# Optimization experiments

Measured on AMD Instinct MI355X. Metric: run time of the kernel, lower is better.

The kernel has to match this reference:

```python
import jax, jax.numpy as jnp
import numpy as np

B, S, D, H = 2, 2048, 1024, 16
DK = D // H


def setup_inputs() -> dict:
    key = jax.random.key(0)
    ks = jax.random.split(key, 6)
    scale = 1.0 / np.sqrt(D)
    return {
        "x": jax.random.normal(ks[0], (B, S, D), dtype=jnp.float32),
        "q": jax.random.normal(ks[1], (B, S, D), dtype=jnp.float32),
        "k": jax.random.normal(ks[2], (B, S, D), dtype=jnp.float32),
        "v": jax.random.normal(ks[3], (B, S, D), dtype=jnp.float32),
        "mask": jnp.ones((B, 1, S, S), dtype=jnp.int32),
        "Wq": jax.random.normal(ks[4], (D, D), dtype=jnp.float32) * scale,
        "Wo": jax.random.normal(ks[5], (D, D), dtype=jnp.float32) * scale,
    }


def reference(x, q, k, v, mask, Wq, Wo):
    b = x.shape[0]
    # NOTE: source projects q, k, v ALL through Wq (Wk/Wv unused in forward).
    def proj(t):
        # [b, s, D] -> [b, H, s, DK]   (nn.Linear: t @ W.T)
        return (t @ Wq.T).reshape(b, -1, H, DK).transpose(0, 2, 1, 3)

    query, key_, value = proj(q), proj(k), proj(v)
    # [b, H, Sq, Sk]
    scores = jnp.einsum("bhqd,bhkd->bhqk", query, key_) / np.sqrt(DK)
    scores = jnp.where(mask == 0, jnp.float32(1e-9), scores)
    attn = jax.nn.softmax(scores, axis=-1)
    out = jnp.einsum("bhqk,bhkd->bhqd", attn, value)  # [b, H, Sq, DK]
    out = out.transpose(0, 2, 1, 3).reshape(b, -1, D)
    return out @ Wo.T
```

## Files before the change

kernel.cpp:

```cpp
#include <hip/hip_runtime.h>

#define SEQ  2048
#define DDIM 1024
#define NH   16
#define DK   64

typedef _Float16 half8  __attribute__((ext_vector_type(8)));
typedef _Float16 half4v __attribute__((ext_vector_type(4)));
typedef float    floatx4 __attribute__((ext_vector_type(4)));

__device__ __forceinline__ void load_lds16(const void* g, void* l) {
  __builtin_amdgcn_global_load_lds(
      (const __attribute__((address_space(1))) void*)g,
      (__attribute__((address_space(3))) void*)l, 16, 0, 0);
}

__device__ __forceinline__ float fast_exp2(float x) {
#if __has_builtin(__builtin_amdgcn_exp2f)
  return __builtin_amdgcn_exp2f(x);
#else
  return exp2f(x);
#endif
}

__global__ __launch_bounds__(256) void cvt_kernel(
    const float* __restrict__ q, const float* __restrict__ k,
    const float* __restrict__ v, const float* __restrict__ Wq,
    const float* __restrict__ Wo, _Float16* __restrict__ ws) {
  long t = (long)blockIdx.x * 256 + threadIdx.x;
  long base = t * 4;
  const float* src;
  long off;
  if (base < 12582912L) {
    int which = (int)(base >> 22);
    src = which == 0 ? q : (which == 1 ? k : v);
    off = base & 4194303L;
  } else if (base < 13631488L) {
    src = Wq; off = base - 12582912L;
  } else {
    src = Wo; off = base - 13631488L;
  }
  float4 f = *(const float4*)(src + off);
  half4v h;
  h[0] = (_Float16)f.x; h[1] = (_Float16)f.y;
  h[2] = (_Float16)f.z; h[3] = (_Float16)f.w;
  *(half4v*)(ws + base) = h;
}

__device__ __forceinline__ void gemm128_core(
    const _Float16* __restrict__ A, const _Float16* __restrict__ B,
    int m0, int n0, _Float16* As, _Float16* Bs, floatx4 (&acc)[4][4]) {
  const int tid = threadIdx.x;
  const int lane = tid & 63, w = tid >> 6;
  const int wm = w >> 1, wn = w & 1;
  const int quad = lane >> 4, l15 = lane & 15;
  const int srow = lane >> 2, schunk = lane & 3;

#pragma unroll
  for (int i = 0; i < 4; ++i)
#pragma unroll
    for (int j = 0; j < 4; ++j)
#pragma unroll
      for (int r = 0; r < 4; ++r) acc[i][j][r] = 0.f;

  for (int k0 = 0; k0 < 1024; k0 += 32) {
    __syncthreads();
#pragma unroll
    for (int ii = 0; ii < 2; ++ii) {
      int rA = w * 32 + ii * 16 + srow;
      load_lds16(A + (long)(m0 + rA) * 1024 + k0 + schunk * 8,
                 As + (w * 32 + ii * 16) * 32);
      load_lds16(B + (long)(n0 + rA) * 1024 + k0 + schunk * 8,
                 Bs + (w * 32 + ii * 16) * 32);
    }
    __syncthreads();
    half8 af[4], bf[4];
#pragma unroll
    for (int f = 0; f < 4; ++f) {
      af[f] = *(const half8*)(As + (wm * 64 + f * 16 + l15) * 32 + quad * 8);
      bf[f] = *(const half8*)(Bs + (wn * 64 + f * 16 + l15) * 32 + quad * 8);
    }
#pragma unroll
    for (int i = 0; i < 4; ++i)
#pragma unroll
      for (int j = 0; j < 4; ++j)
        acc[i][j] = __builtin_amdgcn_mfma_f32_16x16x32_f16(af[i], bf[j],
                                                           acc[i][j], 0, 0, 0);
  }
}

__global__ __launch_bounds__(256) void proj_gemm(
    const _Float16* __restrict__ qkv16, const _Float16* __restrict__ w16,
    _Float16* __restrict__ Qp, _Float16* __restrict__ Kp,
    _Float16* __restrict__ Vt) {
  __shared__ __align__(16) _Float16 As[128 * 32];
  __shared__ __align__(16) _Float16 Bs[128 * 32];
  const int t = blockIdx.z;
  floatx4 acc[4][4];
  const int lane = threadIdx.x & 63, w = threadIdx.x >> 6;
  const int wm = w >> 1, wn = w & 1, quad = lane >> 4, l15 = lane & 15;

  if (t < 2) {
    const int m0 = blockIdx.y * 128, n0 = blockIdx.x * 128;
    gemm128_core(qkv16 + (long)t * 4194304, w16, m0, n0, As, Bs, acc);
#pragma unroll
    for (int i = 0; i < 4; ++i)
#pragma unroll
      for (int j = 0; j < 4; ++j)
#pragma unroll
        for (int r = 0; r < 4; ++r) {
          int m = m0 + wm * 64 + i * 16 + quad * 4 + r;
          int n = n0 + wn * 64 + j * 16 + l15;
          int b = m >> 11, s = m & 2047, h = n >> 6, dk = n & 63;
          long bh = b * NH + h;
          float val = acc[i][j][r];
          if (t == 0)
            Qp[(bh * SEQ + s) * DK + dk] = (_Float16)(val * 0.180336880f);
          else
            Kp[(bh * SEQ + s) * DK + dk] = (_Float16)val;
        }
  } else {
    const int m0 = blockIdx.x * 128, n0 = blockIdx.y * 128;
    gemm128_core(w16, qkv16 + 8388608L, m0, n0, As, Bs, acc);
#pragma unroll
    for (int i = 0; i < 4; ++i)
#pragma unroll
      for (int j = 0; j < 4; ++j)
#pragma unroll
        for (int r = 0; r < 4; ++r) {
          int m = m0 + wm * 64 + i * 16 + quad * 4 + r;
          int n = n0 + wn * 64 + j * 16 + l15;
          int h = m >> 6, dk = m & 63, b = n >> 11, s = n & 2047;
          Vt[(((long)b * NH + h) * DK + dk) * SEQ + s] = (_Float16)acc[i][j][r];
        }
  }
}

__global__ __launch_bounds__(256) void out_gemm(
    const _Float16* __restrict__ Aa, const _Float16* __restrict__ Bw,
    float* __restrict__ C) {
  __shared__ __align__(16) _Float16 As[128 * 32];
  __shared__ __align__(16) _Float16 Bs[128 * 32];
  const int m0 = blockIdx.y * 128, n0 = blockIdx.x * 128;
  floatx4 acc[4][4];
  gemm128_core(Aa, Bw, m0, n0, As, Bs, acc);

  const int lane = threadIdx.x & 63, w = threadIdx.x >> 6;
  const int wm = w >> 1, wn = w & 1, quad = lane >> 4, l15 = lane & 15;
#pragma unroll
  for (int i = 0; i < 4; ++i)
#pragma unroll
    for (int j = 0; j < 4; ++j)
#pragma unroll
      for (int r = 0; r < 4; ++r) {
        int m = m0 + wm * 64 + i * 16 + quad * 4 + r;
        int n = n0 + wn * 64 + j * 16 + l15;
        C[(long)m * 1024 + n] = acc[i][j][r];
      }
}

__global__ __launch_bounds__(256) void attn_kernel(
    const _Float16* __restrict__ Qp, const _Float16* __restrict__ Kp,
    const _Float16* __restrict__ Vt, _Float16* __restrict__ Oa) {
  __shared__ __align__(16) _Float16 smem[4096 * 3 + 4 * 16 * 68];
  _Float16* Qs = smem;
  _Float16* Ks = smem + 4096;
  _Float16* Vs = smem + 8192;
  const int tid = threadIdx.x;
  const int lane = tid & 63, w = tid >> 6;
  _Float16* Ps = smem + 12288 + w * (16 * 68);
  const int quad = lane >> 4, l15 = lane & 15;
  const int rl = lane >> 3, cc = lane & 7;
  const int bh = blockIdx.y;
  const int q0 = blockIdx.x * 64;
  const _Float16* Qb = Qp + (long)bh * (SEQ * DK);
  const _Float16* Kb = Kp + (long)bh * (SEQ * DK);
  const _Float16* Vb = Vt + (long)bh * (DK * SEQ);

#pragma unroll
  for (int ii = 0; ii < 2; ++ii) {
    int row = w * 16 + ii * 8 + rl;
    int gcc = cc ^ (row & 7);
    load_lds16(Qb + (long)(q0 + row) * DK + gcc * 8, Qs + (w * 16 + ii * 8) * 64);
  }
  __syncthreads();

  half8 qf[2];
#pragma unroll
  for (int ks = 0; ks < 2; ++ks) {
    int row = w * 16 + l15;
    int c = (ks * 4 + quad) ^ (row & 7);
    qf[ks] = *(const half8*)(Qs + row * 64 + c * 8);
  }

  floatx4 Oacc[4];
  floatx4 Dacc;
#pragma unroll
  for (int r = 0; r < 4; ++r) Dacc[r] = 0.f;
#pragma unroll
  for (int nt = 0; nt < 4; ++nt)
#pragma unroll
    for (int r = 0; r < 4; ++r) Oacc[nt][r] = 0.f;
  half8 ones;
#pragma unroll
  for (int i = 0; i < 8; ++i) ones[i] = (_Float16)1.0f;

  for (int kt = 0; kt < 32; ++kt) {
    const int k0 = kt * 64;
    __syncthreads();
#pragma unroll
    for (int ii = 0; ii < 2; ++ii) {
      int row = w * 16 + ii * 8 + rl;
      int gcc = cc ^ (row & 7);
      load_lds16(Kb + (long)(k0 + row) * DK + gcc * 8, Ks + (w * 16 + ii * 8) * 64);
      load_lds16(Vb + (long)row * SEQ + k0 + gcc * 8, Vs + (w * 16 + ii * 8) * 64);
    }
    __syncthreads();

    floatx4 Sacc[4];
#pragma unroll
    for (int nt = 0; nt < 4; ++nt)
#pragma unroll
      for (int r = 0; r < 4; ++r) Sacc[nt][r] = 0.f;
#pragma unroll
    for (int nt = 0; nt < 4; ++nt) {
#pragma unroll
      for (int ks = 0; ks < 2; ++ks) {
        int row = nt * 16 + l15;
        int c = (ks * 4 + quad) ^ (row & 7);
        half8 kf = *(const half8*)(Ks + row * 64 + c * 8);
        Sacc[nt] = __builtin_amdgcn_mfma_f32_16x16x32_f16(qf[ks], kf,
                                                          Sacc[nt], 0, 0, 0);
      }
    }

#pragma unroll
    for (int nt = 0; nt < 4; ++nt)
#pragma unroll
      for (int r = 0; r < 4; ++r) {
        float p = fast_exp2(Sacc[nt][r]);
        Ps[(quad * 4 + r) * 68 + nt * 16 + l15] = (_Float16)p;
      }

#pragma unroll
    for (int ks = 0; ks < 2; ++ks) {
      half8 pf = *(const half8*)(Ps + l15 * 68 + ks * 32 + quad * 8);
      Dacc = __builtin_amdgcn_mfma_f32_16x16x32_f16(pf, ones, Dacc, 0, 0, 0);
#pragma unroll
      for (int nt = 0; nt < 4; ++nt) {
        int row = nt * 16 + l15;
        int c = (ks * 4 + quad) ^ (row & 7);
        half8 vf = *(const half8*)(Vs + row * 64 + c * 8);
        Oacc[nt] = __builtin_amdgcn_mfma_f32_16x16x32_f16(pf, vf,
                                                          Oacc[nt], 0, 0, 0);
      }
    }
  }

  const int b = bh >> 4, h = bh & 15;
#pragma unroll
  for (int nt = 0; nt < 4; ++nt)
#pragma unroll
    for (int r = 0; r < 4; ++r) {
      float o = Oacc[nt][r] / Dacc[r];
      int srow = q0 + w * 16 + quad * 4 + r;
      int col = nt * 16 + l15;
      Oa[((long)b * SEQ + srow) * DDIM + h * DK + col] = (_Float16)o;
    }
}

extern "C" void kernel_launch(void* const* d_in, const int* in_sizes, int n_in,
                              void* d_out, int out_size, void* d_ws,
                              size_t ws_size, hipStream_t stream) {
  const float* q  = (const float*)d_in[1];
  const float* k  = (const float*)d_in[2];
  const float* v  = (const float*)d_in[3];
  const float* Wq = (const float*)d_in[5];
  const float* Wo = (const float*)d_in[6];
  float* out = (float*)d_out;

  _Float16* ws     = (_Float16*)d_ws;
  _Float16* qkv16  = ws;
  _Float16* wq16   = ws + 12582912;
  _Float16* wo16   = ws + 13631488;
  _Float16* Qp     = ws + 14680064;
  _Float16* Kp     = ws + 18874368;
  _Float16* Vt     = ws + 23068672;
  _Float16* attn16 = ws + 27262976;

  cvt_kernel<<<14336, 256, 0, stream>>>(q, k, v, Wq, Wo, ws);
  proj_gemm<<<dim3(8, 32, 3), 256, 0, stream>>>(qkv16, wq16, Qp, Kp, Vt);
  attn_kernel<<<dim3(32, 32), 256, 0, stream>>>(Qp, Kp, Vt, attn16);
  out_gemm<<<dim3(8, 32), 256, 0, stream>>>(attn16, wo16, out);
}
```

Baseline: 274.4 us.

## Retile GEMMs to 128x64 and restructure attention to keep P in registers

The projection and output GEMMs move from 128x128 to 128x64 tiles on a flattened 1D grid, doubling block count for better occupancy and load balance. The attention kernel drops to 128 threads, each wave handling 32 query rows. It computes S transposed so the exp'd probabilities feed the PV MFMA straight from registers (16x16x16), which removes the LDS round trip for P and the ones-matrix MFMA for the row sum. The epilogue stages the output through LDS so the global stores are coalesced 16-byte writes. These changes trade extra per-block setup and the removed GEMM B-tile reuse for lower LDS traffic and more parallelism.

```diff
diff --git a/kernel.cpp b/kernel.cpp
--- a/kernel.cpp
+++ b/kernel.cpp
@@ -47,17 +47,16 @@
   *(half4v*)(ws + base) = h;
 }
 
-__device__ __forceinline__ void gemm128_core(
+__device__ __forceinline__ void gemm_128x64_core(
     const _Float16* __restrict__ A, const _Float16* __restrict__ B,
-    int m0, int n0, _Float16* As, _Float16* Bs, floatx4 (&acc)[4][4]) {
+    int m0, int n0, _Float16* As, _Float16* Bs, floatx4 (&acc)[2][4]) {
   const int tid = threadIdx.x;
   const int lane = tid & 63, w = tid >> 6;
-  const int wm = w >> 1, wn = w & 1;
   const int quad = lane >> 4, l15 = lane & 15;
   const int srow = lane >> 2, schunk = lane & 3;
 
 #pragma unroll
-  for (int i = 0; i < 4; ++i)
+  for (int i = 0; i < 2; ++i)
 #pragma unroll
     for (int j = 0; j < 4; ++j)
 #pragma unroll
@@ -70,18 +69,22 @@
       int rA = w * 32 + ii * 16 + srow;
       load_lds16(A + (long)(m0 + rA) * 1024 + k0 + schunk * 8,
                  As + (w * 32 + ii * 16) * 32);
-      load_lds16(B + (long)(n0 + rA) * 1024 + k0 + schunk * 8,
-                 Bs + (w * 32 + ii * 16) * 32);
+    }
+    {
+      int rB = w * 16 + srow;
+      load_lds16(B + (long)(n0 + rB) * 1024 + k0 + schunk * 8,
+                 Bs + (w * 16) * 32);
     }
     __syncthreads();
-    half8 af[4], bf[4];
-#pragma unroll
-    for (int f = 0; f < 4; ++f) {
-      af[f] = *(const half8*)(As + (wm * 64 + f * 16 + l15) * 32 + quad * 8);
-      bf[f] = *(const half8*)(Bs + (wn * 64 + f * 16 + l15) * 32 + quad * 8);
-    }
-#pragma unroll
-    for (int i = 0; i < 4; ++i)
+    half8 af[2], bf[4];
+#pragma unroll
+    for (int i = 0; i < 2; ++i)
+      af[i] = *(const half8*)(As + (w * 32 + i * 16 + l15) * 32 + quad * 8);
+#pragma unroll
+    for (int j = 0; j < 4; ++j)
+      bf[j] = *(const half8*)(Bs + (j * 16 + l15) * 32 + quad * 8);
+#pragma unroll
+    for (int i = 0; i < 2; ++i)
 #pragma unroll
       for (int j = 0; j < 4; ++j)
         acc[i][j] = __builtin_amdgcn_mfma_f32_16x16x32_f16(af[i], bf[j],
@@ -94,23 +97,25 @@
     _Float16* __restrict__ Qp, _Float16* __restrict__ Kp,
     _Float16* __restrict__ Vt) {
   __shared__ __align__(16) _Float16 As[128 * 32];
-  __shared__ __align__(16) _Float16 Bs[128 * 32];
-  const int t = blockIdx.z;
-  floatx4 acc[4][4];
+  __shared__ __align__(16) _Float16 Bs[64 * 32];
+  const int bid = blockIdx.x;
+  floatx4 acc[2][4];
   const int lane = threadIdx.x & 63, w = threadIdx.x >> 6;
-  const int wm = w >> 1, wn = w & 1, quad = lane >> 4, l15 = lane & 15;
-
-  if (t < 2) {
-    const int m0 = blockIdx.y * 128, n0 = blockIdx.x * 128;
-    gemm128_core(qkv16 + (long)t * 4194304, w16, m0, n0, As, Bs, acc);
-#pragma unroll
-    for (int i = 0; i < 4; ++i)
+  const int quad = lane >> 4, l15 = lane & 15;
+
+  if (bid < 1024) {
+    const int t = bid >> 9;
+    const int local = bid & 511;
+    const int m0 = (local >> 4) * 128, n0 = (local & 15) * 64;
+    gemm_128x64_core(qkv16 + (long)t * 4194304, w16, m0, n0, As, Bs, acc);
+#pragma unroll
+    for (int i = 0; i < 2; ++i)
 #pragma unroll
       for (int j = 0; j < 4; ++j)
 #pragma unroll
         for (int r = 0; r < 4; ++r) {
-          int m = m0 + wm * 64 + i * 16 + quad * 4 + r;
-          int n = n0 + wn * 64 + j * 16 + l15;
+          int m = m0 + w * 32 + i * 16 + quad * 4 + r;
+          int n = n0 + j * 16 + l15;
           int b = m >> 11, s = m & 2047, h = n >> 6, dk = n & 63;
           long bh = b * NH + h;
           float val = acc[i][j][r];
@@ -120,16 +125,18 @@
             Kp[(bh * SEQ + s) * DK + dk] = (_Float16)val;
         }
   } else {
-    const int m0 = blockIdx.x * 128, n0 = blockIdx.y * 128;
-    gemm128_core(w16, qkv16 + 8388608L, m0, n0, As, Bs, acc);
-#pragma unroll
-    for (int i = 0; i < 4; ++i)
+    const int local = bid - 1024;
+    const int m0 = (local >> 6) * 128;
+    const int n0 = (local & 63) * 64;
+    gemm_128x64_core(w16, qkv16 + 8388608L, m0, n0, As, Bs, acc);
+#pragma unroll
+    for (int i = 0; i < 2; ++i)
 #pragma unroll
       for (int j = 0; j < 4; ++j)
 #pragma unroll
         for (int r = 0; r < 4; ++r) {
-          int m = m0 + wm * 64 + i * 16 + quad * 4 + r;
-          int n = n0 + wn * 64 + j * 16 + l15;
+          int m = m0 + w * 32 + i * 16 + quad * 4 + r;
+          int n = n0 + j * 16 + l15;
           int h = m >> 6, dk = m & 63, b = n >> 11, s = n & 2047;
           Vt[(((long)b * NH + h) * DK + dk) * SEQ + s] = (_Float16)acc[i][j][r];
         }
@@ -140,35 +147,35 @@
     const _Float16* __restrict__ Aa, const _Float16* __restrict__ Bw,
     float* __restrict__ C) {
   __shared__ __align__(16) _Float16 As[128 * 32];
-  __shared__ __align__(16) _Float16 Bs[128 * 32];
-  const int m0 = blockIdx.y * 128, n0 = blockIdx.x * 128;
-  floatx4 acc[4][4];
-  gemm128_core(Aa, Bw, m0, n0, As, Bs, acc);
+  __shared__ __align__(16) _Float16 Bs[64 * 32];
+  const int bid = blockIdx.x;
+  const int m0 = (bid >> 4) * 128, n0 = (bid & 15) * 64;
+  floatx4 acc[2][4];
+  gemm_128x64_core(Aa, Bw, m0, n0, As, Bs, acc);
 
   const int lane = threadIdx.x & 63, w = threadIdx.x >> 6;
-  const int wm = w >> 1, wn = w & 1, quad = lane >> 4, l15 = lane & 15;
-#pragma unroll
-  for (int i = 0; i < 4; ++i)
+  const int quad = lane >> 4, l15 = lane & 15;
+#pragma unroll
+  for (int i = 0; i < 2; ++i)
 #pragma unroll
     for (int j = 0; j < 4; ++j)
 #pragma unroll
       for (int r = 0; r < 4; ++r) {
-        int m = m0 + wm * 64 + i * 16 + quad * 4 + r;
-        int n = n0 + wn * 64 + j * 16 + l15;
+        int m = m0 + w * 32 + i * 16 + quad * 4 + r;
+        int n = n0 + j * 16 + l15;
         C[(long)m * 1024 + n] = acc[i][j][r];
       }
 }
 
-__global__ __launch_bounds__(256) void attn_kernel(
+__global__ __launch_bounds__(128) void attn_kernel(
     const _Float16* __restrict__ Qp, const _Float16* __restrict__ Kp,
     const _Float16* __restrict__ Vt, _Float16* __restrict__ Oa) {
-  __shared__ __align__(16) _Float16 smem[4096 * 3 + 4 * 16 * 68];
+  __shared__ __align__(16) _Float16 smem[12288];
   _Float16* Qs = smem;
   _Float16* Ks = smem + 4096;
   _Float16* Vs = smem + 8192;
   const int tid = threadIdx.x;
   const int lane = tid & 63, w = tid >> 6;
-  _Float16* Ps = smem + 12288 + w * (16 * 68);
   const int quad = lane >> 4, l15 = lane & 15;
   const int rl = lane >> 3, cc = lane & 7;
   const int bh = blockIdx.y;
@@ -178,95 +185,129 @@
   const _Float16* Vb = Vt + (long)bh * (DK * SEQ);
 
 #pragma unroll
-  for (int ii = 0; ii < 2; ++ii) {
-    int row = w * 16 + ii * 8 + rl;
-    int gcc = cc ^ (row & 7);
-    load_lds16(Qb + (long)(q0 + row) * DK + gcc * 8, Qs + (w * 16 + ii * 8) * 64);
+  for (int ii = 0; ii < 4; ++ii) {
+    int row = w * 32 + ii * 8 + rl;
+    int sw = (cc ^ (row & 7)) * 8;
+    load_lds16(Qb + (long)(q0 + row) * DK + sw, Qs + (w * 32 + ii * 8) * 64);
+  }
+#pragma unroll
+  for (int ii = 0; ii < 4; ++ii) {
+    int row = w * 32 + ii * 8 + rl;
+    int sw = (cc ^ (row & 7)) * 8;
+    load_lds16(Kb + (long)row * DK + sw, Ks + (w * 32 + ii * 8) * 64);
+    load_lds16(Vb + (long)row * SEQ + sw, Vs + (w * 32 + ii * 8) * 64);
   }
   __syncthreads();
 
-  half8 qf[2];
-#pragma unroll
-  for (int ks = 0; ks < 2; ++ks) {
-    int row = w * 16 + l15;
-    int c = (ks * 4 + quad) ^ (row & 7);
-    qf[ks] = *(const half8*)(Qs + row * 64 + c * 8);
-  }
-
-  floatx4 Oacc[4];
-  floatx4 Dacc;
-#pragma unroll
-  for (int r = 0; r < 4; ++r) Dacc[r] = 0.f;
-#pragma unroll
-  for (int nt = 0; nt < 4; ++nt)
-#pragma unroll
-    for (int r = 0; r < 4; ++r) Oacc[nt][r] = 0.f;
-  half8 ones;
-#pragma unroll
-  for (int i = 0; i < 8; ++i) ones[i] = (_Float16)1.0f;
+  half8 qf[2][2];
+#pragma unroll
+  for (int qn = 0; qn < 2; ++qn)
+#pragma unroll
+    for (int ks = 0; ks < 2; ++ks) {
+      int row = w * 32 + qn * 16 + l15;
+      int c = (ks * 4 + quad) ^ (row & 7);
+      qf[qn][ks] = *(const half8*)(Qs + row * 64 + c * 8);
+    }
+
+  floatx4 Oacc[2][4];
+  float den[2] = {0.f, 0.f};
+#pragma unroll
+  for (int qn = 0; qn < 2; ++qn)
+#pragma unroll
+    for (int dt = 0; dt < 4; ++dt)
+#pragma unroll
+      for (int r = 0; r < 4; ++r) Oacc[qn][dt][r] = 0.f;
 
   for (int kt = 0; kt < 32; ++kt) {
-    const int k0 = kt * 64;
-    __syncthreads();
-#pragma unroll
-    for (int ii = 0; ii < 2; ++ii) {
-      int row = w * 16 + ii * 8 + rl;
-      int gcc = cc ^ (row & 7);
-      load_lds16(Kb + (long)(k0 + row) * DK + gcc * 8, Ks + (w * 16 + ii * 8) * 64);
-      load_lds16(Vb + (long)row * SEQ + k0 + gcc * 8, Vs + (w * 16 + ii * 8) * 64);
-    }
-    __syncthreads();
-
-    floatx4 Sacc[4];
-#pragma unroll
-    for (int nt = 0; nt < 4; ++nt)
-#pragma unroll
-      for (int r = 0; r < 4; ++r) Sacc[nt][r] = 0.f;
-#pragma unroll
-    for (int nt = 0; nt < 4; ++nt) {
+    half4v pbf[4][2];
+#pragma unroll
+    for (int mt = 0; mt < 4; ++mt) {
+      floatx4 Sacc[2];
+#pragma unroll
+      for (int qn = 0; qn < 2; ++qn)
+#pragma unroll
+        for (int r = 0; r < 4; ++r) Sacc[qn][r] = 0.f;
 #pragma unroll
       for (int ks = 0; ks < 2; ++ks) {
-        int row = nt * 16 + l15;
+        int row = mt * 16 + l15;
         int c = (ks * 4 + quad) ^ (row & 7);
         half8 kf = *(const half8*)(Ks + row * 64 + c * 8);
-        Sacc[nt] = __builtin_amdgcn_mfma_f32_16x16x32_f16(qf[ks], kf,
-                                                          Sacc[nt], 0, 0, 0);
-      }
-    }
-
-#pragma unroll
-    for (int nt = 0; nt < 4; ++nt)
+#pragma unroll
+        for (int qn = 0; qn < 2; ++qn)
+          Sacc[qn] = __builtin_amdgcn_mfma_f32_16x16x32_f16(kf, qf[qn][ks],
+                                                            Sacc[qn], 0, 0, 0);
+      }
+#pragma unroll
+      for (int qn = 0; qn < 2; ++qn) {
+        float e0 = fast_exp2(Sacc[qn][0]);
+        float e1 = fast_exp2(Sacc[qn][1]);
+        float e2 = fast_exp2(Sacc[qn][2]);
+        float e3 = fast_exp2(Sacc[qn][3]);
+        den[qn] += (e0 + e1) + (e2 + e3);
+        half4v p;
+        p[0] = (_Float16)e0; p[1] = (_Float16)e1;
+        p[2] = (_Float16)e2; p[3] = (_Float16)e3;
+        pbf[mt][qn] = p;
+      }
+    }
+
+#pragma unroll
+    for (int dt = 0; dt < 4; ++dt)
+#pragma unroll
+      for (int mt = 0; mt < 4; ++mt) {
+        int row = dt * 16 + l15;
+        int c8 = mt * 2 + (quad >> 1);
+        half4v vf = *(const half4v*)(Vs + row * 64 + ((c8 ^ (row & 7)) * 8) +
+                                     (quad & 1) * 4);
+#pragma unroll
+        for (int qn = 0; qn < 2; ++qn)
+          Oacc[qn][dt] = __builtin_amdgcn_mfma_f32_16x16x16f16(
+              vf, pbf[mt][qn], Oacc[qn][dt], 0, 0, 0);
+      }
+
+    if (kt < 31) {
+      __syncthreads();
+      const int k0 = (kt + 1) * 64;
+#pragma unroll
+      for (int ii = 0; ii < 4; ++ii) {
+        int row = w * 32 + ii * 8 + rl;
+        int sw = (cc ^ (row & 7)) * 8;
+        load_lds16(Kb + (long)(k0 + row) * DK + sw, Ks + (w * 32 + ii * 8) * 64);
+        load_lds16(Vb + (long)row * SEQ + k0 + sw, Vs + (w * 32 + ii * 8) * 64);
+      }
+      __syncthreads();
+    }
+  }
+
+  float inv[2];
+#pragma unroll
+  for (int qn = 0; qn < 2; ++qn) {
+    float d = den[qn];
+    d += __shfl_xor(d, 16, 64);
+    d += __shfl_xor(d, 32, 64);
+    inv[qn] = __builtin_amdgcn_rcpf(d);
+  }
+
+#pragma unroll
+  for (int qn = 0; qn < 2; ++qn)
+#pragma unroll
+    for (int dt = 0; dt < 4; ++dt)
 #pragma unroll
       for (int r = 0; r < 4; ++r) {
-        float p = fast_exp2(Sacc[nt][r]);
-        Ps[(quad * 4 + r) * 68 + nt * 16 + l15] = (_Float16)p;
-      }
-
-#pragma unroll
-    for (int ks = 0; ks < 2; ++ks) {
-      half8 pf = *(const half8*)(Ps + l15 * 68 + ks * 32 + quad * 8);
-      Dacc = __builtin_amdgcn_mfma_f32_16x16x32_f16(pf, ones, Dacc, 0, 0, 0);
-#pragma unroll
-      for (int nt = 0; nt < 4; ++nt) {
-        int row = nt * 16 + l15;
-        int c = (ks * 4 + quad) ^ (row & 7);
-        half8 vf = *(const half8*)(Vs + row * 64 + c * 8);
-        Oacc[nt] = __builtin_amdgcn_mfma_f32_16x16x32_f16(pf, vf,
-                                                          Oacc[nt], 0, 0, 0);
-      }
-    }
-  }
-
+        int ql = w * 32 + qn * 16 + l15;
+        int c8 = dt * 2 + (quad >> 1);
+        Qs[ql * 64 + ((c8 ^ (ql & 7)) * 8) + (quad & 1) * 4 + r] =
+            (_Float16)(Oacc[qn][dt][r] * inv[qn]);
+      }
+  __syncthreads();
   const int b = bh >> 4, h = bh & 15;
-#pragma unroll
-  for (int nt = 0; nt < 4; ++nt)
-#pragma unroll
-    for (int r = 0; r < 4; ++r) {
-      float o = Oacc[nt][r] / Dacc[r];
-      int srow = q0 + w * 16 + quad * 4 + r;
-      int col = nt * 16 + l15;
-      Oa[((long)b * SEQ + srow) * DDIM + h * DK + col] = (_Float16)o;
-    }
+  const int qloc = tid >> 1, hf = tid & 1;
+#pragma unroll
+  for (int c = 0; c < 4; ++c) {
+    int c8 = hf * 4 + c;
+    half8 val = *(const half8*)(Qs + qloc * 64 + ((c8 ^ (qloc & 7)) * 8));
+    *(half8*)(Oa + ((long)b * SEQ + q0 + qloc) * DDIM + h * DK + c8 * 8) = val;
+  }
 }
 
 extern "C" void kernel_launch(void* const* d_in, const int* in_sizes, int n_in,
@@ -289,7 +330,7 @@
   _Float16* attn16 = ws + 27262976;
 
   cvt_kernel<<<14336, 256, 0, stream>>>(q, k, v, Wq, Wo, ws);
-  proj_gemm<<<dim3(8, 32, 3), 256, 0, stream>>>(qkv16, wq16, Qp, Kp, Vt);
-  attn_kernel<<<dim3(32, 32), 256, 0, stream>>>(Qp, Kp, Vt, attn16);
-  out_gemm<<<dim3(8, 32), 256, 0, stream>>>(attn16, wo16, out);
-}
+  proj_gemm<<<1536, 256, 0, stream>>>(qkv16, wq16, Qp, Kp, Vt);
+  attn_kernel<<<dim3(32, 32), 128, 0, stream>>>(Qp, Kp, Vt, attn16);
+  out_gemm<<<512, 256, 0, stream>>>(attn16, wo16, out);
+}
```

After: 269.7 us. No clear change (-1.7%).
